# Kernel optimization log

Hardware: AMD Instinct MI355X
Metric: run time of the kernel (lower is better)

## Reference

```python
import jax, jax.numpy as jnp
import numpy as np

N, E, D, H = 50000, 800000, 128, 4
DH = D // H  # head dim = 32


def setup_inputs() -> dict:
    key = jax.random.key(0)
    ks = jax.random.split(key, 16)
    inp = {
        "node_feats": jax.random.normal(ks[0], (N, D), jnp.float32),
        "edge_feats": jax.random.normal(ks[1], (E, D), jnp.float32),
        "src": jax.random.randint(ks[2], (E,), 0, N, jnp.int32),
        "dst": jax.random.randint(ks[3], (E,), 0, N, jnp.int32),
        # MHA projections (no bias since num_input == num_output feats)
        "Wq": jax.random.normal(ks[4], (D, D), jnp.float32) / np.sqrt(D),
        "Wk": jax.random.normal(ks[5], (D, D), jnp.float32) / np.sqrt(D),
        "Wv": jax.random.normal(ks[6], (D, D), jnp.float32) / np.sqrt(D),
        "We": jax.random.normal(ks[7], (D, D), jnp.float32) / np.sqrt(D),
        # output projection (with bias)
        "O_w": jax.random.normal(ks[8], (D, D), jnp.float32) / np.sqrt(D),
        "O_b": jnp.zeros((D,), jnp.float32),
        # batch-norm affine params
        "g1n": jnp.ones((D,), jnp.float32), "b1n": jnp.zeros((D,), jnp.float32),
        "g1e": jnp.ones((D,), jnp.float32), "b1e": jnp.zeros((D,), jnp.float32),
        "g2": jnp.ones((D,), jnp.float32), "b2": jnp.zeros((D,), jnp.float32),
        # node-feats MLP (no bias)
        "W1": jax.random.normal(ks[9], (D, 2 * D), jnp.float32) / np.sqrt(D),
        "W2": jax.random.normal(ks[10], (2 * D, D), jnp.float32) / np.sqrt(2 * D),
    }
    return inp


def _batch_norm(x, gamma, beta, eps=1e-5):
    # training-style BatchNorm1d: biased variance over the batch (node/edge) dim
    mean = jnp.mean(x, axis=0)
    var = jnp.var(x, axis=0)
    return (x - mean) * jax.lax.rsqrt(var + eps) * gamma + beta


def reference(node_feats, edge_feats, src, dst, Wq, Wk, Wv, We, O_w, O_b,
              g1n, b1n, g1e, b1e, g2, b2, W1, W2):
    h_in1 = node_feats
    nf = _batch_norm(node_feats, g1n, b1n)
    ef = _batch_norm(edge_feats, g1e, b1e)

    Q = (nf @ Wq).reshape(N, H, DH)
    K = (nf @ Wk).reshape(N, H, DH)
    V = (nf @ Wv).reshape(N, H, DH)
    proj_e = (ef @ We).reshape(E, H, DH)

    # edge-wise multiplicative attention: [E, H, DH]
    score = jnp.clip(K[src] * Q[dst] / np.sqrt(DH).astype(np.float32), -5.0, 5.0) * proj_e
    s = jnp.exp(jnp.clip(jnp.sum(score, axis=-1, keepdims=True), -5.0, 5.0))  # [E, H, 1]

    # scatter-sum aggregation to destination nodes
    wV = jax.ops.segment_sum(s * V[src], dst, num_segments=N)  # [N, H, DH]
    z = jax.ops.segment_sum(s, dst, num_segments=N)            # [N, H, 1]
    h = (wV / (z + 1e-6)).reshape(N, D)

    # dropout is identity in eval mode
    h = h @ O_w + O_b
    h = h_in1 + h  # residual 1

    h_in2 = h
    h = _batch_norm(h, g2, b2)
    h = jax.nn.silu(h @ W1) @ W2  # node_feats_MLP (dropout = identity)
    h = h_in2 + h  # residual 2
    return h
```

## Files before the change

### kernel.cpp

```cpp
#include <hip/hip_runtime.h>
#include <hip/hip_bf16.h>
#include <math.h>

#define N_NODES 50000
#define N_EDGES 800000
#define DIM 128
#define NH 4

typedef __attribute__((ext_vector_type(8))) short bf16x8;
typedef __attribute__((ext_vector_type(4))) float f32x4;
typedef unsigned int uint;
typedef unsigned short ushort;

__device__ inline short f2bf(float f) {
  __hip_bfloat16 h = __float2bfloat16(f);
  return __builtin_bit_cast(short, h);
}
__device__ inline uint pack_bf2(float lo, float hi) {
  return (uint)(ushort)f2bf(lo) | ((uint)(ushort)f2bf(hi) << 16);
}
__device__ inline float bflo(uint u) { return __builtin_bit_cast(float, u << 16); }
__device__ inline float bfhi(uint u) { return __builtin_bit_cast(float, u & 0xffff0000u); }

__global__ __launch_bounds__(256) void stats_all_kernel(
    const float* __restrict__ nf, const float* __restrict__ ef,
    const int* __restrict__ dst,
    float* __restrict__ stats_n, float* __restrict__ stats_e,
    int* __restrict__ deg, ushort* __restrict__ efb) {
  __shared__ float s_sum[DIM];
  __shared__ float s_sq[DIM];
  int t = threadIdx.x;
  if (t < DIM) { s_sum[t] = 0.f; s_sq[t] = 0.f; }
  __syncthreads();
  int c4 = (t & 31) * 4;
  int rg = t >> 5;
  float sum0=0,sum1=0,sum2=0,sum3=0, sq0=0,sq1=0,sq2=0,sq3=0;
  if (blockIdx.x < 512) {
    for (long row = (long)blockIdx.x * 8 + rg; row < N_NODES; row += 512L * 8) {
      float4 v = *reinterpret_cast<const float4*>(nf + row * DIM + c4);
      sum0 += v.x; sq0 += v.x * v.x;
      sum1 += v.y; sq1 += v.y * v.y;
      sum2 += v.z; sq2 += v.z * v.z;
      sum3 += v.w; sq3 += v.w * v.w;
    }
    atomicAdd(&s_sum[c4 + 0], sum0); atomicAdd(&s_sq[c4 + 0], sq0);
    atomicAdd(&s_sum[c4 + 1], sum1); atomicAdd(&s_sq[c4 + 1], sq1);
    atomicAdd(&s_sum[c4 + 2], sum2); atomicAdd(&s_sq[c4 + 2], sq2);
    atomicAdd(&s_sum[c4 + 3], sum3); atomicAdd(&s_sq[c4 + 3], sq3);
    __syncthreads();
    if (t < DIM) {
      atomicAdd(&stats_n[t], s_sum[t]);
      atomicAdd(&stats_n[DIM + t], s_sq[t]);
    }
  } else {
    long bid2 = blockIdx.x - 512;
    for (long i = bid2 * 256 + t; i < N_EDGES; i += 2048L * 256) {
      atomicAdd(&deg[dst[i]], 1);
    }
    for (long row = bid2 * 8 + rg; row < N_EDGES; row += 2048L * 8) {
      float4 v = *reinterpret_cast<const float4*>(ef + row * DIM + c4);
      sum0 += v.x; sq0 += v.x * v.x;
      sum1 += v.y; sq1 += v.y * v.y;
      sum2 += v.z; sq2 += v.z * v.z;
      sum3 += v.w; sq3 += v.w * v.w;
      uint2 p;
      p.x = pack_bf2(v.x, v.y);
      p.y = pack_bf2(v.z, v.w);
      *reinterpret_cast<uint2*>(efb + row * DIM + c4) = p;
    }
    atomicAdd(&s_sum[c4 + 0], sum0); atomicAdd(&s_sq[c4 + 0], sq0);
    atomicAdd(&s_sum[c4 + 1], sum1); atomicAdd(&s_sq[c4 + 1], sq1);
    atomicAdd(&s_sum[c4 + 2], sum2); atomicAdd(&s_sq[c4 + 2], sq2);
    atomicAdd(&s_sum[c4 + 3], sum3); atomicAdd(&s_sq[c4 + 3], sq3);
    __syncthreads();
    if (t < DIM) {
      atomicAdd(&stats_e[t], s_sum[t]);
      atomicAdd(&stats_e[DIM + t], s_sq[t]);
    }
  }
}

#define SCAN_T 1024
#define PER_T 49
__global__ __launch_bounds__(1024) void fold7_kernel(
    const float* __restrict__ Wq, const float* __restrict__ Wk,
    const float* __restrict__ Wv, const float* __restrict__ We,
    const float* __restrict__ Ow, const float* __restrict__ W2,
    const float* __restrict__ stats_n, const float* __restrict__ stats_e,
    const float* __restrict__ g1n, const float* __restrict__ b1n,
    const float* __restrict__ g1e, const float* __restrict__ b1e, float inv_s,
    short* __restrict__ WqT, short* __restrict__ WkT,
    short* __restrict__ WvT, short* __restrict__ WeT,
    short* __restrict__ OwT, short* __restrict__ W2T,
    float* __restrict__ bq, float* __restrict__ bk,
    float* __restrict__ bv, float* __restrict__ be,
    const int* __restrict__ deg, int* __restrict__ row_start,
    int* __restrict__ cursor) {
  int b = blockIdx.x;
  int t = threadIdx.x;
  if (b == 6) {
    __shared__ int ps[SCAN_T];
    int base = t * PER_T;
    int lsum = 0;
    int local[PER_T];
#pragma unroll
    for (int j = 0; j < PER_T; ++j) {
      int idx = base + j;
      int d = (idx < N_NODES) ? deg[idx] : 0;
      local[j] = lsum;
      lsum += d;
    }
    ps[t] = lsum;
    __syncthreads();
    for (int off = 1; off < SCAN_T; off <<= 1) {
      int v = (t >= off) ? ps[t - off] : 0;
      __syncthreads();
      ps[t] += v;
      __syncthreads();
    }
    int prefix = (t == 0) ? 0 : ps[t - 1];
#pragma unroll
    for (int j = 0; j < PER_T; ++j) {
      int idx = base + j;
      if (idx < N_NODES) {
        int v = prefix + local[j];
        row_start[idx] = v;
        cursor[idx] = v;
      }
    }
    if (t == SCAN_T - 1) row_start[N_NODES] = ps[SCAN_T - 1];
    return;
  }
  if (b == 4) {
    int d = t & 127, kg = t >> 7;
#pragma unroll
    for (int j = 0; j < 16; ++j) {
      int k = kg * 16 + j;
      OwT[d * DIM + k] = f2bf(Ow[k * DIM + d]);
    }
    return;
  }
  if (b == 5) {
    int d = t & 127, kg = t >> 7;
#pragma unroll
    for (int j = 0; j < 32; ++j) {
      int k = kg * 32 + j;
      W2T[d * 256 + k] = f2bf(W2[k * DIM + d]);
    }
    return;
  }
  __shared__ float red[8][DIM];
  __shared__ float sab[DIM], sbb[DIM];
  const float* W = (b == 0) ? Wq : (b == 1) ? Wk : (b == 2) ? Wv : We;
  const float* stats = (b == 3) ? stats_e : stats_n;
  const float* gamma = (b == 3) ? g1e : g1n;
  const float* beta  = (b == 3) ? b1e : b1n;
  float M            = (b == 3) ? (float)N_EDGES : (float)N_NODES;
  float scale = (b == 1) ? inv_s : 1.f;
  short* WT = (b == 0) ? WqT : (b == 1) ? WkT : (b == 2) ? WvT : WeT;
  float* bias = (b == 0) ? bq : (b == 1) ? bk : (b == 2) ? bv : be;
  if (t < DIM) {
    float mean = stats[t] / M;
    float var = stats[DIM + t] / M - mean * mean;
    float a = gamma[t] * rsqrtf(var + 1e-5f);
    sab[t] = a;
    sbb[t] = beta[t] - mean * a;
  }
  __syncthreads();
  int d = t & 127, kg = t >> 7;
  int ct = d >> 4, lr = d & 15;
  int L = (ct >> 1) * 32 + lr * 2 + (ct & 1);
  float bacc = 0.f;
#pragma unroll
  for (int j = 0; j < 16; ++j) {
    int k = kg * 16 + j;
    float wv = W[k * DIM + L];
    WT[d * DIM + k] = f2bf(scale * sab[k] * wv);
    bacc += sbb[k] * wv;
  }
  red[kg][d] = bacc;
  __syncthreads();
  if (kg == 0) {
    float s = 0.f;
#pragma unroll
    for (int j = 0; j < 8; ++j) s += red[j][d];
    bias[d] = scale * s;
  }
}

__global__ __launch_bounds__(256) void fold_w1_kernel(
    const float* __restrict__ W1, const float* __restrict__ stats_h,
    const float* __restrict__ g2, const float* __restrict__ b2,
    short* __restrict__ W1F, float* __restrict__ bias1) {
  __shared__ float sab[DIM], sbb[DIM];
  __shared__ float red[16][17];
  int t = threadIdx.x;
  if (t < DIM) {
    float mean = stats_h[t] / (float)N_NODES;
    float var = stats_h[DIM + t] / (float)N_NODES - mean * mean;
    float a = g2[t] * rsqrtf(var + 1e-5f);
    sab[t] = a;
    sbb[t] = b2[t] - mean * a;
  }
  __syncthreads();
  int dl = t & 15, kg = t >> 4;
  int d = blockIdx.x * 16 + dl;
  float bacc = 0.f;
#pragma unroll
  for (int j = 0; j < 8; ++j) {
    int k = kg * 8 + j;
    float wv = W1[k * 256 + d];
    W1F[d * DIM + k] = f2bf(sab[k] * wv);
    bacc += sbb[k] * wv;
  }
  red[dl][kg] = bacc;
  __syncthreads();
  if (kg == 0) {
    float s = 0.f;
#pragma unroll
    for (int j = 0; j < 16; ++j) s += red[dl][j];
    bias1[d] = s;
  }
}

__device__ inline void load_a_frags(const float* __restrict__ X, long m0,
                                    int lr, int lg, bf16x8 a[4]) {
#pragma unroll
  for (int ks = 0; ks < 4; ++ks) {
    const float* p = X + (m0 + lr) * DIM + ks * 32 + lg * 8;
    float4 v0 = *reinterpret_cast<const float4*>(p);
    float4 v1 = *reinterpret_cast<const float4*>(p + 4);
    bf16x8 af;
    af[0] = f2bf(v0.x); af[1] = f2bf(v0.y); af[2] = f2bf(v0.z); af[3] = f2bf(v0.w);
    af[4] = f2bf(v1.x); af[5] = f2bf(v1.y); af[6] = f2bf(v1.z); af[7] = f2bf(v1.w);
    a[ks] = af;
  }
}

#define QKV_BLOCKS 782
__global__ __launch_bounds__(256) void scatter_qkv_kernel(
    const float* __restrict__ nf,
    const short* __restrict__ WqT, const short* __restrict__ WkT, const short* __restrict__ WvT,
    const float* __restrict__ bq, const float* __restrict__ bk, const float* __restrict__ bv,
    ushort* __restrict__ Qb, ushort* __restrict__ Kb, ushort* __restrict__ Vb,
    const int* __restrict__ src, const int* __restrict__ dst,
    int* __restrict__ cursor, int2* __restrict__ csr) {
  int t = threadIdx.x;
  if (blockIdx.x >= QKV_BLOCKS) {
    int i = (blockIdx.x - QKV_BLOCKS) * 256 + t;
    int d = dst[i];
    int pos = atomicAdd(&cursor[d], 1);
    csr[pos] = make_int2(src[i], i);
    return;
  }
  int w = t >> 6, l = t & 63;
  int lr = l & 15, lg = l >> 4;
  long m0 = (long)blockIdx.x * 64 + w * 16;
  if (m0 >= N_NODES) return;
  bf16x8 a[4];
  load_a_frags(nf, m0, lr, lg, a);
  const short* Ws[3] = {WqT, WkT, WvT};
  const float* bs[3] = {bq, bk, bv};
  ushort* Os[3] = {Qb, Kb, Vb};
#pragma unroll 1
  for (int m = 0; m < 3; ++m) {
    const short* WT = Ws[m];
    f32x4 acc[8];
#pragma unroll
    for (int ct = 0; ct < 8; ++ct) acc[ct] = (f32x4){0.f, 0.f, 0.f, 0.f};
#pragma unroll
    for (int ct = 0; ct < 8; ++ct) {
#pragma unroll
      for (int ks = 0; ks < 4; ++ks) {
        bf16x8 b = *reinterpret_cast<const bf16x8*>(WT + (ct * 16 + lr) * DIM + ks * 32 + lg * 8);
        acc[ct] = __builtin_amdgcn_mfma_f32_16x16x32_bf16(a[ks], b, acc[ct], 0, 0, 0);
      }
    }
    const float* bb = bs[m];
    ushort* O = Os[m];
#pragma unroll
    for (int h = 0; h < 4; ++h) {
      float b0 = bb[(2 * h) * 16 + lr];
      float b1 = bb[(2 * h + 1) * 16 + lr];
#pragma unroll
      for (int r = 0; r < 4; ++r) {
        uint u = pack_bf2(acc[2 * h][r] + b0, acc[2 * h + 1][r] + b1);
        *reinterpret_cast<uint*>(O + (m0 + lg * 4 + r) * DIM + h * 32 + lr * 2) = u;
      }
    }
  }
}

#define ES_GRID 2048
__global__ __launch_bounds__(256) void edge_score_kernel(
    const ushort* __restrict__ efb,
    const int* __restrict__ src, const int* __restrict__ dst,
    const short* __restrict__ WeT, const float* __restrict__ be,
    const ushort* __restrict__ Qb, const ushort* __restrict__ Kb,
    float* __restrict__ s_out) {
  const int NT = N_EDGES / 64;
  int t = threadIdx.x;
  int w = t >> 6, l = t & 63;
  int lr = l & 15, lg = l >> 4;
  float ber[8];
#pragma unroll
  for (int ct = 0; ct < 8; ++ct) ber[ct] = be[ct * 16 + lr];

  for (int tile = blockIdx.x; tile < NT; tile += gridDim.x) {
    long m0 = (long)tile * 64 + w * 16;
    long eb = m0 + lg * 4;
    int4 s4 = *reinterpret_cast<const int4*>(src + eb);
    int4 d4 = *reinterpret_cast<const int4*>(dst + eb);
    int sn[4] = {s4.x, s4.y, s4.z, s4.w};
    int dn[4] = {d4.x, d4.y, d4.z, d4.w};
    uint Kg[4][4], Qg[4][4];
#pragma unroll
    for (int r = 0; r < 4; ++r) {
#pragma unroll
      for (int h = 0; h < 4; ++h) {
        Kg[r][h] = *reinterpret_cast<const uint*>(Kb + (long)sn[r] * DIM + h * 32 + lr * 2);
        Qg[r][h] = *reinterpret_cast<const uint*>(Qb + (long)dn[r] * DIM + h * 32 + lr * 2);
      }
    }
    bf16x8 a[4];
#pragma unroll
    for (int ks = 0; ks < 4; ++ks) {
      a[ks] = __builtin_nontemporal_load(
          reinterpret_cast<const bf16x8*>(efb + (m0 + lr) * DIM + ks * 32 + lg * 8));
    }
    f32x4 acc[8];
#pragma unroll
    for (int ct = 0; ct < 8; ++ct) acc[ct] = (f32x4){0.f, 0.f, 0.f, 0.f};
    __builtin_amdgcn_s_setprio(1);
#pragma unroll
    for (int ct = 0; ct < 8; ++ct) {
#pragma unroll
      for (int ks = 0; ks < 4; ++ks) {
        bf16x8 b = *reinterpret_cast<const bf16x8*>(WeT + (ct * 16 + lr) * DIM + ks * 32 + lg * 8);
        acc[ct] = __builtin_amdgcn_mfma_f32_16x16x32_bf16(a[ks], b, acc[ct], 0, 0, 0);
      }
    }
    __builtin_amdgcn_s_setprio(0);
#pragma unroll
    for (int r = 0; r < 4; ++r) {
      float hs0, hs1, hs2, hs3;
      {
        float h0, h1, h2, h3;
#pragma unroll
        for (int h = 0; h < 4; ++h) {
          float k0 = bflo(Kg[r][h]), k1 = bfhi(Kg[r][h]);
          float q0 = bflo(Qg[r][h]), q1 = bfhi(Qg[r][h]);
          float pe0 = acc[2 * h][r] + ber[2 * h];
          float pe1 = acc[2 * h + 1][r] + ber[2 * h + 1];
          float v = fminf(fmaxf(k0 * q0, -5.f), 5.f) * pe0
                  + fminf(fmaxf(k1 * q1, -5.f), 5.f) * pe1;
          if (h == 0) h0 = v; else if (h == 1) h1 = v; else if (h == 2) h2 = v; else h3 = v;
        }
        hs0 = h0; hs1 = h1; hs2 = h2; hs3 = h3;
      }
#pragma unroll
      for (int m2 = 8; m2 >= 1; m2 >>= 1) {
        hs0 += __shfl_xor(hs0, m2);
        hs1 += __shfl_xor(hs1, m2);
        hs2 += __shfl_xor(hs2, m2);
        hs3 += __shfl_xor(hs3, m2);
      }
      if (lr < 4) {
        float myh = (lr == 0) ? hs0 : ((lr == 1) ? hs1 : ((lr == 2) ? hs2 : hs3));
        s_out[(eb + r) * 4 + lr] = __expf(fminf(fmaxf(myh, -5.f), 5.f));
      }
    }
  }
}

__global__ __launch_bounds__(256) void aggregate_kernel(
    const int* __restrict__ row_start, const int2* __restrict__ csr,
    const float* __restrict__ s_arr, const ushort* __restrict__ Vb,
    ushort* __restrict__ haggb) {
  int t = threadIdx.x;
  int w = t >> 6, l = t & 63;
  int n = blockIdx.x * 4 + w;
  int r0 = row_start[n], r1 = row_start[n + 1];
  int h = l >> 4;
  float a0 = 0.f, a1 = 0.f, zacc = 0.f;
  int idx = r0;
  for (; idx + 4 <= r1; idx += 4) {
    int2 rec[4];
#pragma unroll
    for (int j = 0; j < 4; ++j) rec[j] = csr[idx + j];
    float sv[4]; uint uv[4];
#pragma unroll
    for (int j = 0; j < 4; ++j) {
      sv[j] = s_arr[(long)rec[j].y * 4 + h];
      uv[j] = *reinterpret_cast<const uint*>(Vb + (long)rec[j].x * DIM + l * 2);
    }
#pragma unroll
    for (int j = 0; j < 4; ++j) {
      a0 += sv[j] * bflo(uv[j]);
      a1 += sv[j] * bfhi(uv[j]);
      zacc += sv[j];
    }
  }
  for (; idx < r1; ++idx) {
    int2 ra = csr[idx];
    float sa = s_arr[(long)ra.y * 4 + h];
    uint ua = *reinterpret_cast<const uint*>(Vb + (long)ra.x * DIM + l * 2);
    a0 += sa * bflo(ua);
    a1 += sa * bfhi(ua);
    zacc += sa;
  }
  float inv = 1.f / (zacc + 1e-6f);
  *reinterpret_cast<uint*>(haggb + (long)n * DIM + l * 2) = pack_bf2(a0 * inv, a1 * inv);
}

__global__ __launch_bounds__(256) void attnout_mfma_kernel(
    const ushort* __restrict__ haggb, const short* __restrict__ OwT,
    const float* __restrict__ Ob, const float* __restrict__ h_in1,
    float* __restrict__ hres, float* __restrict__ stats2) {
  int t = threadIdx.x;
  int w = t >> 6, l = t & 63;
  int lr = l & 15, lg = l >> 4;
  long m0 = (long)blockIdx.x * 64 + w * 16;
  if (m0 >= N_NODES) return;
  bf16x8 a[4];
#pragma unroll
  for (int ks = 0; ks < 4; ++ks) {
    a[ks] = *reinterpret_cast<const bf16x8*>(haggb + (m0 + lr) * DIM + ks * 32 + lg * 8);
  }
  f32x4 acc[8];
#pragma unroll
  for (int ct = 0; ct < 8; ++ct) acc[ct] = (f32x4){0.f, 0.f, 0.f, 0.f};
#pragma unroll
  for (int ct = 0; ct < 8; ++ct) {
#pragma unroll
    for (int ks = 0; ks < 4; ++ks) {
      bf16x8 b = *reinterpret_cast<const bf16x8*>(OwT + (ct * 16 + lr) * DIM + ks * 32 + lg * 8);
      acc[ct] = __builtin_amdgcn_mfma_f32_16x16x32_bf16(a[ks], b, acc[ct], 0, 0, 0);
    }
  }
#pragma unroll
  for (int ct = 0; ct < 8; ++ct) {
    float ob = Ob[ct * 16 + lr];
    float ls = 0.f, lq = 0.f;
#pragma unroll
    for (int r = 0; r < 4; ++r) {
      long idx = (m0 + lg * 4 + r) * DIM + ct * 16 + lr;
      float hv = h_in1[idx] + acc[ct][r] + ob;
      hres[idx] = hv;
      ls += hv; lq += hv * hv;
    }
    ls += __shfl_xor(ls, 16); ls += __shfl_xor(ls, 32);
    lq += __shfl_xor(lq, 16); lq += __shfl_xor(lq, 32);
    if (lg == 0) {
      atomicAdd(&stats2[ct * 16 + lr], ls);
      atomicAdd(&stats2[DIM + ct * 16 + lr], lq);
    }
  }
}

__global__ __launch_bounds__(256) void mlp_mfma_kernel(
    const float* __restrict__ hres, const short* __restrict__ W1F,
    const float* __restrict__ bias1, const short* __restrict__ W2T,
    float* __restrict__ out) {
  __shared__ short mid[64][264];
  int t = threadIdx.x;
  int w = t >> 6, l = t & 63;
  int lr = l & 15, lg = l >> 4;
  long m0 = (long)blockIdx.x * 64 + w * 16;
  if (m0 >= N_NODES) return;
  bf16x8 a1[4];
  load_a_frags(hres, m0, lr, lg, a1);
#pragma unroll
  for (int ct = 0; ct < 16; ++ct) {
    f32x4 acc = (f32x4){0.f, 0.f, 0.f, 0.f};
#pragma unroll
    for (int ks = 0; ks < 4; ++ks) {
      bf16x8 b = *reinterpret_cast<const bf16x8*>(W1F + (ct * 16 + lr) * DIM + ks * 32 + lg * 8);
      acc = __builtin_amdgcn_mfma_f32_16x16x32_bf16(a1[ks], b, acc, 0, 0, 0);
    }
    float bb = bias1[ct * 16 + lr];
#pragma unroll
    for (int r = 0; r < 4; ++r) {
      float x = acc[r] + bb;
      float sl = x / (1.f + __expf(-x));
      mid[w * 16 + lg * 4 + r][ct * 16 + lr] = f2bf(sl);
    }
  }
  bf16x8 a2[8];
#pragma unroll
  for (int ks = 0; ks < 8; ++ks) {
    a2[ks] = *reinterpret_cast<const bf16x8*>(&mid[w * 16 + lr][ks * 32 + lg * 8]);
  }
#pragma unroll
  for (int ct = 0; ct < 8; ++ct) {
    f32x4 acc = (f32x4){0.f, 0.f, 0.f, 0.f};
#pragma unroll
    for (int ks = 0; ks < 8; ++ks) {
      bf16x8 b = *reinterpret_cast<const bf16x8*>(W2T + (ct * 16 + lr) * 256 + ks * 32 + lg * 8);
      acc = __builtin_amdgcn_mfma_f32_16x16x32_bf16(a2[ks], b, acc, 0, 0, 0);
    }
#pragma unroll
    for (int r = 0; r < 4; ++r) {
      long idx = (m0 + lg * 4 + r) * DIM + ct * 16 + lr;
      out[idx] = hres[idx] + acc[r];
    }
  }
}

extern "C" void kernel_launch(void* const* d_in, const int* in_sizes, int n_in,
                              void* d_out, int out_size, void* d_ws, size_t ws_size,
                              hipStream_t stream) {
  const float* node_feats = (const float*)d_in[0];
  const float* edge_feats = (const float*)d_in[1];
  const int* src = (const int*)d_in[2];
  const int* dst = (const int*)d_in[3];
  const float* Wq = (const float*)d_in[4];
  const float* Wk = (const float*)d_in[5];
  const float* Wv = (const float*)d_in[6];
  const float* We = (const float*)d_in[7];
  const float* Ow = (const float*)d_in[8];
  const float* Ob = (const float*)d_in[9];
  const float* g1n = (const float*)d_in[10];
  const float* b1n = (const float*)d_in[11];
  const float* g1e = (const float*)d_in[12];
  const float* b1e = (const float*)d_in[13];
  const float* g2 = (const float*)d_in[14];
  const float* b2 = (const float*)d_in[15];
  const float* W1 = (const float*)d_in[16];
  const float* W2 = (const float*)d_in[17];
  float* out = (float*)d_out;
  float* w = (float*)d_ws;

  float* stats_n = w + 0;
  float* stats_e = w + 256;
  float* stats_h = w + 512;
  float* bq = w + 1536;
  float* bk = w + 1664;
  float* bv = w + 1792;
  float* be = w + 1920;
  short* WqT = (short*)(w + 2048);
  short* WkT = (short*)(w + 10240);
  short* WvT = (short*)(w + 18432);
  short* WeT = (short*)(w + 26624);
  short* OwT = (short*)(w + 34816);
  short* W1F = (short*)(w + 43008);
  short* W2T = (short*)(w + 59392);
  float* bias1 = w + 75776;
  ushort* Qb = (ushort*)(w + 76032);
  ushort* Kb = (ushort*)(w + 3276032);
  ushort* Vb = (ushort*)(w + 6476032);
  float* s_arr = w + 9676032;
  int* deg = (int*)(w + 12876032);
  int* row_start = deg + 50048;
  int* cursor = row_start + 50064;
  int2* csr = (int2*)(cursor + 50048);
  ushort* efb = (ushort*)(w + 16226192);
  ushort* haggb = (ushort*)(w + 76032);

  const float inv_s = 0.17677669529663687f;

  hipMemsetAsync(w, 0, 768 * sizeof(float), stream);
  hipMemsetAsync(deg, 0, 50000 * sizeof(int), stream);

  stats_all_kernel<<<2560, 256, 0, stream>>>(
      node_feats, edge_feats, dst, stats_n, stats_e, deg, efb);
  fold7_kernel<<<7, 1024, 0, stream>>>(Wq, Wk, Wv, We, Ow, W2, stats_n, stats_e,
                                       g1n, b1n, g1e, b1e, inv_s,
                                       WqT, WkT, WvT, WeT, OwT, W2T, bq, bk, bv, be,
                                       deg, row_start, cursor);
  scatter_qkv_kernel<<<QKV_BLOCKS + N_EDGES / 256, 256, 0, stream>>>(
      node_feats, WqT, WkT, WvT, bq, bk, bv, Qb, Kb, Vb, src, dst, cursor, csr);
  edge_score_kernel<<<ES_GRID, 256, 0, stream>>>(
      efb, src, dst, WeT, be, Qb, Kb, s_arr);
  aggregate_kernel<<<N_NODES / 4, 256, 0, stream>>>(row_start, csr, s_arr, Vb, haggb);
  attnout_mfma_kernel<<<(N_NODES + 63) / 64, 256, 0, stream>>>(
      haggb, OwT, Ob, node_feats, out, stats_h);
  fold_w1_kernel<<<16, 256, 0, stream>>>(W1, stats_h, g2, b2, W1F, bias1);
  mlp_mfma_kernel<<<(N_NODES + 63) / 64, 256, 0, stream>>>(out, W1F, bias1, W2T, out);
}
```

Before: 732.5 us.

## Pack edge scores to bf16, widen aggregate unroll, merge memsets, add setprio

Edge attention scores are now stored as four packed bf16 values per edge (8 bytes) instead of four fp32 values, which halves the traffic for both writing and gathering them. The aggregate loop is unrolled 8 deep instead of 4 so more gathers are in flight at once. The stats buffers are moved next to the degree array so a single memset clears both, and s_setprio is placed around the MFMA loop in the QKV kernel. The cost is lower precision in the attention weights and more register pressure in the aggregate kernel.

```diff
diff --git a/kernel.cpp b/kernel.cpp
--- a/kernel.cpp
+++ b/kernel.cpp
@@ -268,6 +268,7 @@
     f32x4 acc[8];
 #pragma unroll
     for (int ct = 0; ct < 8; ++ct) acc[ct] = (f32x4){0.f, 0.f, 0.f, 0.f};
+    __builtin_amdgcn_s_setprio(1);
 #pragma unroll
     for (int ct = 0; ct < 8; ++ct) {
 #pragma unroll
@@ -276,6 +277,7 @@
         acc[ct] = __builtin_amdgcn_mfma_f32_16x16x32_bf16(a[ks], b, acc[ct], 0, 0, 0);
       }
     }
+    __builtin_amdgcn_s_setprio(0);
     const float* bb = bs[m];
     ushort* O = Os[m];
 #pragma unroll
@@ -297,7 +299,7 @@
     const int* __restrict__ src, const int* __restrict__ dst,
     const short* __restrict__ WeT, const float* __restrict__ be,
     const ushort* __restrict__ Qb, const ushort* __restrict__ Kb,
-    float* __restrict__ s_out) {
+    uint2* __restrict__ s_pack) {
   const int NT = N_EDGES / 64;
   int t = threadIdx.x;
   int w = t >> 6, l = t & 63;
@@ -365,9 +367,15 @@
         hs2 += __shfl_xor(hs2, m2);
         hs3 += __shfl_xor(hs3, m2);
       }
-      if (lr < 4) {
-        float myh = (lr == 0) ? hs0 : ((lr == 1) ? hs1 : ((lr == 2) ? hs2 : hs3));
-        s_out[(eb + r) * 4 + lr] = __expf(fminf(fmaxf(myh, -5.f), 5.f));
+      if (lr == 0) {
+        float e0 = __expf(fminf(fmaxf(hs0, -5.f), 5.f));
+        float e1 = __expf(fminf(fmaxf(hs1, -5.f), 5.f));
+        float e2 = __expf(fminf(fmaxf(hs2, -5.f), 5.f));
+        float e3 = __expf(fminf(fmaxf(hs3, -5.f), 5.f));
+        uint2 p;
+        p.x = pack_bf2(e0, e1);
+        p.y = pack_bf2(e2, e3);
+        s_pack[eb + r] = p;
       }
     }
   }
@@ -375,7 +383,7 @@
 
 __global__ __launch_bounds__(256) void aggregate_kernel(
     const int* __restrict__ row_start, const int2* __restrict__ csr,
-    const float* __restrict__ s_arr, const ushort* __restrict__ Vb,
+    const uint2* __restrict__ s_pack, const ushort* __restrict__ Vb,
     ushort* __restrict__ haggb) {
   int t = threadIdx.x;
   int w = t >> 6, l = t & 63;
@@ -384,18 +392,20 @@
   int h = l >> 4;
   float a0 = 0.f, a1 = 0.f, zacc = 0.f;
   int idx = r0;
-  for (; idx + 4 <= r1; idx += 4) {
-    int2 rec[4];
-#pragma unroll
-    for (int j = 0; j < 4; ++j) rec[j] = csr[idx + j];
-    float sv[4]; uint uv[4];
-#pragma unroll
-    for (int j = 0; j < 4; ++j) {
-      sv[j] = s_arr[(long)rec[j].y * 4 + h];
+  for (; idx + 8 <= r1; idx += 8) {
+    int2 rec[8];
+#pragma unroll
+    for (int j = 0; j < 8; ++j) rec[j] = csr[idx + j];
+    float sv[8]; uint uv[8];
+#pragma unroll
+    for (int j = 0; j < 8; ++j) {
+      uint2 sp = s_pack[rec[j].y];
+      uint uw = (h < 2) ? sp.x : sp.y;
+      sv[j] = (h & 1) ? bfhi(uw) : bflo(uw);
       uv[j] = *reinterpret_cast<const uint*>(Vb + (long)rec[j].x * DIM + l * 2);
     }
 #pragma unroll
-    for (int j = 0; j < 4; ++j) {
+    for (int j = 0; j < 8; ++j) {
       a0 += sv[j] * bflo(uv[j]);
       a1 += sv[j] * bfhi(uv[j]);
       zacc += sv[j];
@@ -403,7 +413,9 @@
   }
   for (; idx < r1; ++idx) {
     int2 ra = csr[idx];
-    float sa = s_arr[(long)ra.y * 4 + h];
+    uint2 sp = s_pack[ra.y];
+    uint uw = (h < 2) ? sp.x : sp.y;
+    float sa = (h & 1) ? bfhi(uw) : bflo(uw);
     uint ua = *reinterpret_cast<const uint*>(Vb + (long)ra.x * DIM + l * 2);
     a0 += sa * bflo(ua);
     a1 += sa * bfhi(ua);
@@ -531,9 +543,6 @@
   float* out = (float*)d_out;
   float* w = (float*)d_ws;
 
-  float* stats_n = w + 0;
-  float* stats_e = w + 256;
-  float* stats_h = w + 512;
   float* bq = w + 1536;
   float* bk = w + 1664;
   float* bv = w + 1792;
@@ -549,18 +558,20 @@
   ushort* Qb = (ushort*)(w + 76032);
   ushort* Kb = (ushort*)(w + 3276032);
   ushort* Vb = (ushort*)(w + 6476032);
-  float* s_arr = w + 9676032;
+  uint2* s_pack = (uint2*)(w + 9676032);
   int* deg = (int*)(w + 12876032);
-  int* row_start = deg + 50048;
+  float* stats_n = w + 12926080;
+  float* stats_e = stats_n + 256;
+  float* stats_h = stats_e + 256;
+  int* row_start = (int*)(stats_h + 256);
   int* cursor = row_start + 50064;
   int2* csr = (int2*)(cursor + 50048);
-  ushort* efb = (ushort*)(w + 16226192);
+  ushort* efb = (ushort*)(w + 16227008);
   ushort* haggb = (ushort*)(w + 76032);
 
   const float inv_s = 0.17677669529663687f;
 
-  hipMemsetAsync(w, 0, 768 * sizeof(float), stream);
-  hipMemsetAsync(deg, 0, 50000 * sizeof(int), stream);
+  hipMemsetAsync(deg, 0, (50048 + 768) * sizeof(int), stream);
 
   stats_all_kernel<<<2560, 256, 0, stream>>>(
       node_feats, edge_feats, dst, stats_n, stats_e, deg, efb);
@@ -571,8 +582,8 @@
   scatter_qkv_kernel<<<QKV_BLOCKS + N_EDGES / 256, 256, 0, stream>>>(
       node_feats, WqT, WkT, WvT, bq, bk, bv, Qb, Kb, Vb, src, dst, cursor, csr);
   edge_score_kernel<<<ES_GRID, 256, 0, stream>>>(
-      efb, src, dst, WeT, be, Qb, Kb, s_arr);
-  aggregate_kernel<<<N_NODES / 4, 256, 0, stream>>>(row_start, csr, s_arr, Vb, haggb);
+      efb, src, dst, WeT, be, Qb, Kb, s_pack);
+  aggregate_kernel<<<N_NODES / 4, 256, 0, stream>>>(row_start, csr, s_pack, Vb, haggb);
   attnout_mfma_kernel<<<(N_NODES + 63) / 64, 256, 0, stream>>>(
       haggb, OwT, Ob, node_feats, out, stats_h);
   fold_w1_kernel<<<16, 256, 0, stream>>>(W1, stats_h, g2, b2, W1F, bias1);
```

New measurement: 715.5 us. 1.02x faster.
